# Kernel tuning notes

Hardware: AMD Instinct MI355X
Metric: run time of the kernel (lower is better)

Reference implementation:

```python
import jax, jax.numpy as jnp
import numpy as np

DIM, WIDTH, TOTAL, BATCH, NSLOTS = 4096, 4, 16384, 8, 256


def setup_inputs() -> dict:
    key = jax.random.key(0)
    ks = jax.random.split(key, 6)
    x = jax.random.normal(ks[0], (DIM, TOTAL), dtype=jnp.float32)
    weight = jax.random.normal(ks[1], (DIM, WIDTH), dtype=jnp.float32) * 0.1
    conv_states = jax.random.normal(ks[2], (NSLOTS, DIM, WIDTH - 1), dtype=jnp.float32)
    cuts = jnp.sort(jax.random.randint(ks[3], (BATCH - 1,), 1, TOTAL)).astype(jnp.int32)
    query_start_loc = jnp.concatenate([
        jnp.zeros((1,), jnp.int32), cuts, jnp.full((1,), TOTAL, jnp.int32)])
    cache_indices = jax.random.permutation(ks[4], NSLOTS)[:BATCH].astype(jnp.int32)
    initial_state_mode = jax.random.randint(ks[5], (BATCH,), 0, 2).astype(jnp.int32)
    return dict(x=x, weight=weight, conv_states=conv_states,
                query_start_loc=query_start_loc, cache_indices=cache_indices,
                initial_state_mode=initial_state_mode,
                pad_slot_id=-1, residual_connection=1)


def _causal_conv1d_varlen(x, weight, conv_states, qsl, cache_indices, init_mode,
                          pad_slot_id, residual_connection):
    dim, T = x.shape
    width = weight.shape[1]
    state_len = width - 1
    nslots = conv_states.shape[0]
    B = qsl.shape[0] - 1

    t = jnp.arange(T)
    # sequence id and local position of every packed token
    seg = jnp.clip(jnp.searchsorted(qsl, t, side='right') - 1, 0, B - 1)  # [T]
    p = t - qsl[seg]                                                      # [T] local pos
    raw_slot = cache_indices[seg]
    valid_slot = raw_slot != pad_slot_id
    slot = jnp.where(valid_slot, raw_slot, 0)
    use_init = (init_mode[seg] != 0) & valid_slot                         # [T]

    # depthwise causal conv: out[:,t] = sum_k w[:,k] * concat(init_state, x_seq)[:, p+k]
    out = jnp.zeros_like(x)
    for k in range(width):
        d = width - 1 - k  # lookback distance
        if d == 0:
            val = x
        else:
            in_seq = p >= d
            vx = x[:, jnp.clip(t - d, 0, T - 1)]                          # [dim,T]
            st_idx = jnp.clip(state_len - d + p, 0, state_len - 1)        # [T]
            vs = conv_states[slot, :, st_idx].T                           # [dim,T]
            val = jnp.where(in_seq[None, :], vx,
                            jnp.where(use_init[None, :], vs, 0.0))
        out = out + weight[:, k:k + 1] * val

    if residual_connection:
        out = out + x

    # updated cache: last state_len entries of concat(init_state, x_seq) per sequence
    j = jnp.arange(state_len)                                             # [S]
    start, end = qsl[:-1], qsl[1:]
    L = end - start                                                       # [B]
    gx = end[:, None] + j[None, :] - state_len                            # [B,S] global idx
    from_x = gx >= start[:, None]                                         # [B,S]
    sidx = jnp.clip(L[:, None] + j[None, :], 0, state_len - 1)            # [B,S]
    b_valid = cache_indices != pad_slot_id
    b_slot = jnp.where(b_valid, cache_indices, 0)
    b_init = (init_mode != 0) & b_valid
    vx_new = x[:, jnp.clip(gx, 0, T - 1)]                                 # [dim,B,S]
    vs_new = jnp.transpose(conv_states[b_slot[:, None], :, sidx], (2, 0, 1))  # [dim,B,S]
    init_vals = jnp.where(b_init[None, :, None], vs_new, 0.0)
    new_states = jnp.where(from_x[None, :, :], vx_new, init_vals)         # [dim,B,S]
    new_states = jnp.transpose(new_states, (1, 0, 2))                     # [B,dim,S]

    # scatter (pad_slot_id rows go to a throwaway extra slot)
    cs_ext = jnp.concatenate(
        [conv_states, jnp.zeros((1, dim, state_len), conv_states.dtype)], axis=0)
    scatter_idx = jnp.where(b_valid, cache_indices, nslots)
    cs_ext = cs_ext.at[scatter_idx].set(new_states)
    return out, cs_ext[:nslots]


def reference(x, weight, conv_states, query_start_loc, cache_indices,
              initial_state_mode, pad_slot_id, residual_connection):
    return _causal_conv1d_varlen(x, weight, conv_states, query_start_loc,
                                 cache_indices, initial_state_mode,
                                 pad_slot_id, residual_connection)
```

## Files before the change

### kernel.cpp

```cpp
#include <hip/hip_runtime.h>

#define DIM 4096
#define TOTAL 16384
#define WIDTH 4
#define STATE_LEN 3
#define BATCH 8
#define NSLOTS 256
#define TVEC (TOTAL / 4)
#define NCONV_BLK ((DIM * TVEC) / 256)
#define SROW (DIM * STATE_LEN)
#define S4_PER_SLOT (SROW / 4)
#define NSTATE4 (NSLOTS * S4_PER_SLOT)
#define NSTATE_BLK (NSTATE4 / 256)

typedef float floatx4 __attribute__((ext_vector_type(4)));

__global__ __launch_bounds__(256) void fused_kernel(
    const float* __restrict__ x, const float* __restrict__ weight,
    const float* __restrict__ cs, const int* __restrict__ qsl,
    const int* __restrict__ cache_indices, const int* __restrict__ init_mode,
    const int* __restrict__ pad_p, const int* __restrict__ res_p,
    float* __restrict__ out, float* __restrict__ out_states)
{
    __shared__ int s_qsl[BATCH + 1];
    __shared__ int s_ci[BATCH];
    __shared__ int s_im[BATCH];
    __shared__ int s_map[NSLOTS];
    __shared__ int s_pad, s_res;

    if (blockIdx.x < NCONV_BLK) {
        if (threadIdx.x < BATCH + 1) s_qsl[threadIdx.x] = qsl[threadIdx.x];
        if (threadIdx.x >= 32 && threadIdx.x < 32 + BATCH) s_ci[threadIdx.x - 32] = cache_indices[threadIdx.x - 32];
        if (threadIdx.x >= 64 && threadIdx.x < 64 + BATCH) s_im[threadIdx.x - 64] = init_mode[threadIdx.x - 64];
        if (threadIdx.x == 96) s_pad = pad_p[0];
        if (threadIdx.x == 97) s_res = res_p[0];
        __syncthreads();

        unsigned v = blockIdx.x * 256u + threadIdx.x;
        int d  = v >> 12;
        int tv = v & (TVEC - 1);
        int t0 = tv << 2;

        const floatx4* xr = (const floatx4*)(x + (size_t)d * TOTAL);
        floatx4 cur = xr[tv];
        floatx4 prev = (floatx4){0.f, 0.f, 0.f, 0.f};
        if (tv > 0) prev = xr[tv - 1];
        float win[7] = {prev.y, prev.z, prev.w, cur.x, cur.y, cur.z, cur.w};

        floatx4 w = ((const floatx4*)weight)[d];
        if (s_res) w.w += 1.0f;

        int seg = 0;
        float res4[4];
        #pragma unroll
        for (int i = 0; i < 4; i++) {
            int t = t0 + i;
            while (seg + 1 < BATCH && t >= s_qsl[seg + 1]) seg++;
            int p = t - s_qsl[seg];
            float xt = win[3 + i];
            float acc;
            if (p >= 3) {
                acc = w.x * win[i] + w.y * win[i + 1] + w.z * win[i + 2] + w.w * xt;
            } else {
                int raw = s_ci[seg];
                bool valid = (raw != s_pad);
                int slot = valid ? raw : 0;
                bool use_init = valid && (s_im[seg] != 0);
                const float* csrow = cs + ((size_t)slot * DIM + d) * STATE_LEN;
                float xm1 = (p >= 1) ? win[i + 2] : (use_init ? csrow[2 + p] : 0.f);
                float xm2 = (p >= 2) ? win[i + 1] : (use_init ? csrow[1 + p] : 0.f);
                float xm3 =                          (use_init ? csrow[0 + p] : 0.f);
                acc = w.x * xm3 + w.y * xm2 + w.z * xm1 + w.w * xt;
            }
            res4[i] = acc;
        }
        floatx4 rv = (floatx4){res4[0], res4[1], res4[2], res4[3]};
        __builtin_nontemporal_store(rv, (floatx4*)(out + (size_t)d * TOTAL) + tv);
    } else {
        s_map[threadIdx.x] = -1;
        if (threadIdx.x < BATCH + 1) s_qsl[threadIdx.x] = qsl[threadIdx.x];
        if (threadIdx.x >= 32 && threadIdx.x < 32 + BATCH) s_im[threadIdx.x - 32] = init_mode[threadIdx.x - 32];
        __syncthreads();
        if (threadIdx.x < BATCH) {
            int raw = cache_indices[threadIdx.x];
            if (raw != pad_p[0] && raw >= 0 && raw < NSLOTS) s_map[raw] = threadIdx.x;
        }
        __syncthreads();

        int f = (blockIdx.x - NCONV_BLK) * 256 + threadIdx.x;
        int slot = f / S4_PER_SLOT;
        int r4   = f - slot * S4_PER_SLOT;
        int b = s_map[slot];
        floatx4 cv = ((const floatx4*)cs)[f];
        if (b < 0) {
            __builtin_nontemporal_store(cv, (floatx4*)out_states + f);
        } else {
            int start = s_qsl[b], end = s_qsl[b + 1];
            int L = end - start;
            bool init = (s_im[b] != 0);
            int base = r4 * 4;
            float r[4];
            #pragma unroll
            for (int e = 0; e < 4; e++) {
                int idx = base + e;
                int d = idx / 3;
                int j = idx - d * 3;
                int gx = end + j - STATE_LEN;
                float val;
                if (gx >= start) {
                    val = x[(size_t)d * TOTAL + gx];
                } else if (init) {
                    int sidx = L + j;
                    if (sidx > STATE_LEN - 1) sidx = STATE_LEN - 1;
                    val = cs[(size_t)slot * SROW + (idx - j) + sidx];
                } else {
                    val = 0.f;
                }
                r[e] = val;
            }
            floatx4 rv = (floatx4){r[0], r[1], r[2], r[3]};
            __builtin_nontemporal_store(rv, (floatx4*)out_states + f);
        }
    }
}

extern "C" void kernel_launch(void* const* d_in, const int* in_sizes, int n_in,
                              void* d_out, int out_size, void* d_ws, size_t ws_size,
                              hipStream_t stream) {
    const float* x      = (const float*)d_in[0];
    const float* weight = (const float*)d_in[1];
    const float* cs     = (const float*)d_in[2];
    const int*   qsl    = (const int*)d_in[3];
    const int*   ci     = (const int*)d_in[4];
    const int*   im     = (const int*)d_in[5];
    const int*   pad    = (const int*)d_in[6];
    const int*   res    = (const int*)d_in[7];

    float* out        = (float*)d_out;
    float* out_states = out + (size_t)DIM * TOTAL;

    fused_kernel<<<NCONV_BLK + NSTATE_BLK, 256, 0, stream>>>(
        x, weight, cs, qsl, ci, im, pad, res, out, out_states);
}
```

Measured before the change: 499.4 us.

## Use persistent grid-stride loops with register-held metadata and fast interior path

Replaces the one-block-per-tile launch (~66k+ blocks) with a fixed 2048-block grid in which each thread loops over state-copy and conv work. The batch metadata is loaded into registers per thread instead of shared memory, which removes the __syncthreads barriers. A branchless segment-boundary check sends tiles wholly inside a sequence to a straight 4-output FMA path. The aim is less block launch and scheduling overhead and less divergence on a bandwidth-bound kernel. The cost is per-thread scalar loads of the metadata and a serialized state phase ahead of the conv phase in each thread.

```diff
diff --git a/kernel.cpp b/kernel.cpp
--- a/kernel.cpp
+++ b/kernel.cpp
@@ -2,16 +2,16 @@
 
 #define DIM 4096
 #define TOTAL 16384
-#define WIDTH 4
 #define STATE_LEN 3
 #define BATCH 8
 #define NSLOTS 256
 #define TVEC (TOTAL / 4)
-#define NCONV_BLK ((DIM * TVEC) / 256)
+#define NCONV4 (DIM * TVEC)
 #define SROW (DIM * STATE_LEN)
 #define S4_PER_SLOT (SROW / 4)
 #define NSTATE4 (NSLOTS * S4_PER_SLOT)
-#define NSTATE_BLK (NSTATE4 / 256)
+#define NBLK 2048
+#define NTHREADS (NBLK * 256)
 
 typedef float floatx4 __attribute__((ext_vector_type(4)));
 
@@ -22,83 +22,37 @@
     const int* __restrict__ pad_p, const int* __restrict__ res_p,
     float* __restrict__ out, float* __restrict__ out_states)
 {
-    __shared__ int s_qsl[BATCH + 1];
-    __shared__ int s_ci[BATCH];
-    __shared__ int s_im[BATCH];
-    __shared__ int s_map[NSLOTS];
-    __shared__ int s_pad, s_res;
+    int q[BATCH + 1];
+    #pragma unroll
+    for (int k = 0; k <= BATCH; k++) q[k] = qsl[k];
+    int ci_[BATCH], im_[BATCH];
+    #pragma unroll
+    for (int k = 0; k < BATCH; k++) { ci_[k] = cache_indices[k]; im_[k] = init_mode[k]; }
+    const int pad = pad_p[0];
+    const float wres = res_p[0] ? 1.0f : 0.0f;
 
-    if (blockIdx.x < NCONV_BLK) {
-        if (threadIdx.x < BATCH + 1) s_qsl[threadIdx.x] = qsl[threadIdx.x];
-        if (threadIdx.x >= 32 && threadIdx.x < 32 + BATCH) s_ci[threadIdx.x - 32] = cache_indices[threadIdx.x - 32];
-        if (threadIdx.x >= 64 && threadIdx.x < 64 + BATCH) s_im[threadIdx.x - 64] = init_mode[threadIdx.x - 64];
-        if (threadIdx.x == 96) s_pad = pad_p[0];
-        if (threadIdx.x == 97) s_res = res_p[0];
-        __syncthreads();
+    const int tid = blockIdx.x * 256 + threadIdx.x;
+    const floatx4* __restrict__ x4 = (const floatx4*)x;
+    const floatx4* __restrict__ cs4 = (const floatx4*)cs;
 
-        unsigned v = blockIdx.x * 256u + threadIdx.x;
-        int d  = v >> 12;
-        int tv = v & (TVEC - 1);
-        int t0 = tv << 2;
-
-        const floatx4* xr = (const floatx4*)(x + (size_t)d * TOTAL);
-        floatx4 cur = xr[tv];
-        floatx4 prev = (floatx4){0.f, 0.f, 0.f, 0.f};
-        if (tv > 0) prev = xr[tv - 1];
-        float win[7] = {prev.y, prev.z, prev.w, cur.x, cur.y, cur.z, cur.w};
-
-        floatx4 w = ((const floatx4*)weight)[d];
-        if (s_res) w.w += 1.0f;
-
-        int seg = 0;
-        float res4[4];
+    for (int f = tid; f < NSTATE4; f += NTHREADS) {
+        int slot = f / S4_PER_SLOT;
+        floatx4 cv = cs4[f];
+        bool found = false; int start = 0, end = 0, imv = 0;
         #pragma unroll
-        for (int i = 0; i < 4; i++) {
-            int t = t0 + i;
-            while (seg + 1 < BATCH && t >= s_qsl[seg + 1]) seg++;
-            int p = t - s_qsl[seg];
-            float xt = win[3 + i];
-            float acc;
-            if (p >= 3) {
-                acc = w.x * win[i] + w.y * win[i + 1] + w.z * win[i + 2] + w.w * xt;
-            } else {
-                int raw = s_ci[seg];
-                bool valid = (raw != s_pad);
-                int slot = valid ? raw : 0;
-                bool use_init = valid && (s_im[seg] != 0);
-                const float* csrow = cs + ((size_t)slot * DIM + d) * STATE_LEN;
-                float xm1 = (p >= 1) ? win[i + 2] : (use_init ? csrow[2 + p] : 0.f);
-                float xm2 = (p >= 2) ? win[i + 1] : (use_init ? csrow[1 + p] : 0.f);
-                float xm3 =                          (use_init ? csrow[0 + p] : 0.f);
-                acc = w.x * xm3 + w.y * xm2 + w.z * xm1 + w.w * xt;
-            }
-            res4[i] = acc;
+        for (int k = 0; k < BATCH; k++) {
+            bool m = (ci_[k] == slot) && (ci_[k] != pad);
+            start = m ? q[k] : start;
+            end   = m ? q[k + 1] : end;
+            imv   = m ? im_[k] : imv;
+            found = found || m;
         }
-        floatx4 rv = (floatx4){res4[0], res4[1], res4[2], res4[3]};
-        __builtin_nontemporal_store(rv, (floatx4*)(out + (size_t)d * TOTAL) + tv);
-    } else {
-        s_map[threadIdx.x] = -1;
-        if (threadIdx.x < BATCH + 1) s_qsl[threadIdx.x] = qsl[threadIdx.x];
-        if (threadIdx.x >= 32 && threadIdx.x < 32 + BATCH) s_im[threadIdx.x - 32] = init_mode[threadIdx.x - 32];
-        __syncthreads();
-        if (threadIdx.x < BATCH) {
-            int raw = cache_indices[threadIdx.x];
-            if (raw != pad_p[0] && raw >= 0 && raw < NSLOTS) s_map[raw] = threadIdx.x;
-        }
-        __syncthreads();
-
-        int f = (blockIdx.x - NCONV_BLK) * 256 + threadIdx.x;
-        int slot = f / S4_PER_SLOT;
-        int r4   = f - slot * S4_PER_SLOT;
-        int b = s_map[slot];
-        floatx4 cv = ((const floatx4*)cs)[f];
-        if (b < 0) {
+        if (!found) {
             __builtin_nontemporal_store(cv, (floatx4*)out_states + f);
         } else {
-            int start = s_qsl[b], end = s_qsl[b + 1];
             int L = end - start;
-            bool init = (s_im[b] != 0);
-            int base = r4 * 4;
+            bool init = (imv != 0);
+            int base = (f - slot * S4_PER_SLOT) * 4;
             float r[4];
             #pragma unroll
             for (int e = 0; e < 4; e++) {
@@ -112,7 +66,7 @@
                 } else if (init) {
                     int sidx = L + j;
                     if (sidx > STATE_LEN - 1) sidx = STATE_LEN - 1;
-                    val = cs[(size_t)slot * SROW + (idx - j) + sidx];
+                    val = cs[(size_t)slot * SROW + d * STATE_LEN + sidx];
                 } else {
                     val = 0.f;
                 }
@@ -121,6 +75,70 @@
             floatx4 rv = (floatx4){r[0], r[1], r[2], r[3]};
             __builtin_nontemporal_store(rv, (floatx4*)out_states + f);
         }
+    }
+
+    #pragma unroll 2
+    for (int v = tid; v < NCONV4; v += NTHREADS) {
+        int d  = v >> 12;
+        int tv = v & (TVEC - 1);
+        int t0 = tv << 2;
+
+        floatx4 cur = x4[v];
+        int pv = (tv > 0) ? (v - 1) : v;
+        floatx4 prev = x4[pv];
+        if (tv == 0) prev = (floatx4){0.f, 0.f, 0.f, 0.f};
+
+        floatx4 w = ((const floatx4*)weight)[d];
+        w.w += wres;
+
+        float win[7] = {prev.y, prev.z, prev.w, cur.x, cur.y, cur.z, cur.w};
+
+        int qs_lo = 0, qs_hi = 0;
+        #pragma unroll
+        for (int k = 1; k < BATCH; k++) {
+            qs_lo = (t0     >= q[k]) ? q[k] : qs_lo;
+            qs_hi = (t0 + 3 >= q[k]) ? q[k] : qs_hi;
+        }
+
+        floatx4 o;
+        if ((qs_lo == qs_hi) && (t0 - qs_lo >= 3)) {
+            o.x = w.x * win[0] + w.y * win[1] + w.z * win[2] + w.w * win[3];
+            o.y = w.x * win[1] + w.y * win[2] + w.z * win[3] + w.w * win[4];
+            o.z = w.x * win[2] + w.y * win[3] + w.z * win[4] + w.w * win[5];
+            o.w = w.x * win[3] + w.y * win[4] + w.z * win[5] + w.w * win[6];
+        } else {
+            float res4[4];
+            #pragma unroll
+            for (int ii = 0; ii < 4; ii++) {
+                int t = t0 + ii;
+                int qs = 0, civ = ci_[0], imv = im_[0];
+                #pragma unroll
+                for (int k = 1; k < BATCH; k++) {
+                    bool m = (t >= q[k]);
+                    qs  = m ? q[k]   : qs;
+                    civ = m ? ci_[k] : civ;
+                    imv = m ? im_[k] : imv;
+                }
+                int p = t - qs;
+                float xt = win[3 + ii];
+                float acc;
+                if (p >= 3) {
+                    acc = w.x * win[ii] + w.y * win[ii + 1] + w.z * win[ii + 2] + w.w * xt;
+                } else {
+                    bool valid = (civ != pad);
+                    int slot = valid ? civ : 0;
+                    bool use_init = valid && (imv != 0);
+                    const float* csrow = cs + ((size_t)slot * DIM + d) * STATE_LEN;
+                    float xm1 = (p >= 1) ? win[ii + 2] : (use_init ? csrow[2 + p] : 0.f);
+                    float xm2 = (p >= 2) ? win[ii + 1] : (use_init ? csrow[1 + p] : 0.f);
+                    float xm3 =                          (use_init ? csrow[0 + p] : 0.f);
+                    acc = w.x * xm3 + w.y * xm2 + w.z * xm1 + w.w * xt;
+                }
+                res4[ii] = acc;
+            }
+            o = (floatx4){res4[0], res4[1], res4[2], res4[3]};
+        }
+        __builtin_nontemporal_store(o, (floatx4*)out + v);
     }
 }
 
@@ -139,6 +157,6 @@
     float* out        = (float*)d_out;
     float* out_states = out + (size_t)DIM * TOTAL;
 
-    fused_kernel<<<NCONV_BLK + NSTATE_BLK, 256, 0, stream>>>(
+    fused_kernel<<<NBLK, 256, 0, stream>>>(
         x, weight, cs, qsl, ci, im, pad, res, out, out_states);
 }
```

After: 516.2 us. +3.4%, slower.
